# Kernel tuning notes

Hardware: AMD Instinct MI355X
Metric: run time of the kernel (lower is better)

## Reference

```python
import jax, jax.numpy as jnp
import numpy as np

NUM_CLASSES = 100000   # vocab (input_dim of the layer)
DIM = 256              # embedding dim (output_dim of the layer)
BATCH = 256
NUM_TRUE = 1024        # hardcoded num_true in call()
NUM_SAMPLED = 16384    # hardcoded num_sampled in call()
LOG_RANGE = float(np.log(NUM_CLASSES + 1.0))


def _sample_log_uniform_unique(rng, n, range_max):
    # Mimics tf log_uniform_candidate_sampler with unique=True: rejection-sample
    # from P(c) ~ log((c+2)/(c+1)) until n unique ids are collected.
    seen = {}
    log_range = np.log(range_max + 1.0)
    while len(seen) < n:
        u = rng.uniform(0.0, log_range, size=2 * n)
        ids = np.minimum(np.floor(np.exp(u) - 1.0).astype(np.int64), range_max - 1)
        for v in ids.tolist():
            if len(seen) >= n:
                break
            seen[v] = None
    return np.fromiter(seen.keys(), dtype=np.int64, count=n)


def setup_inputs() -> dict:
    key = jax.random.key(0)
    k1, k2, k3, k4 = jax.random.split(key, 4)
    inputs = jax.random.normal(k1, (BATCH, DIM), jnp.float32)
    # Original inits w/b to zeros; use small random values for a non-degenerate baseline.
    w = jax.random.normal(k2, (NUM_CLASSES, DIM), jnp.float32) * 0.02
    b = jax.random.normal(k3, (NUM_CLASSES,), jnp.float32) * 0.02
    labels = jax.random.randint(k4, (BATCH, NUM_TRUE), 0, NUM_CLASSES, dtype=jnp.int32)
    rng = np.random.default_rng(0)
    sampled = jnp.asarray(_sample_log_uniform_unique(rng, NUM_SAMPLED, NUM_CLASSES), jnp.int32)
    return {"inputs": inputs, "w": w, "b": b, "labels": labels, "sampled": sampled}


def _log_uniform_prob(ids):
    idf = ids.astype(jnp.float32)
    return jnp.log((idf + 2.0) / (idf + 1.0)) / LOG_RANGE


def _expected_count(ids):
    # P(id appears among NUM_SAMPLED unique candidates) = 1 - (1-p)^NUM_SAMPLED
    p = _log_uniform_prob(ids)
    return -jnp.expm1(NUM_SAMPLED * jnp.log1p(-p))


def _sigmoid_xent(logits, target):
    # numerically stable sigmoid cross-entropy, target is a scalar label value
    return jnp.maximum(logits, 0.0) - logits * target + jnp.log1p(jnp.exp(-jnp.abs(logits)))


def reference(inputs, w, b, labels, sampled):
    # true logits: per-example dot with each true class row  [B, T]
    true_w = w[labels]                                    # [B, T, D] gather
    true_logits = jnp.einsum('bd,btd->bt', inputs, true_w) + b[labels]
    true_logits = true_logits - jnp.log(_expected_count(labels))
    # sampled logits: shared candidate set  [B, S]
    sampled_logits = inputs @ w[sampled].T + b[sampled]
    sampled_logits = sampled_logits - jnp.log(_expected_count(sampled))
    # NCE targets: 1/num_true for true classes, 0 for sampled; sum over columns
    true_xent = _sigmoid_xent(true_logits, 1.0 / NUM_TRUE)
    sampled_xent = _sigmoid_xent(sampled_logits, 0.0)
    return true_xent.sum(axis=1) + sampled_xent.sum(axis=1)   # [B]
```

## Files before the change

### kernel.cpp

```cpp
#include <hip/hip_runtime.h>
#include <hip/hip_bf16.h>

#define NUM_CLASSES 100000
#define DIM 256
#define BATCH 256
#define NUM_TRUE 1024
#define NUM_SAMPLED 16384
#define LOG_RANGE 11.51293546492023f
#define INV_LOG_RANGE (1.0f / LOG_RANGE)

typedef __bf16 bf16x8 __attribute__((ext_vector_type(8)));
typedef float  f32x4  __attribute__((ext_vector_type(4)));

static __device__ __forceinline__ unsigned short f2bf(float f) {
    unsigned int u = __float_as_uint(f);
    unsigned int lsb = (u >> 16) & 1u;
    u += 0x7fffu + lsb;
    return (unsigned short)(u >> 16);
}

static __device__ __forceinline__ float neg_log_ec(int id) {
    float idf = (float)id;
    float p = logf((idf + 2.0f) / (idf + 1.0f)) * INV_LOG_RANGE;
    float ec = -expm1f((float)NUM_SAMPLED * log1pf(-p));
    return -logf(ec);
}

static __device__ __forceinline__ float dot4(float4 a, float4 b) {
    return fmaf(a.x, b.x, fmaf(a.y, b.y, fmaf(a.z, b.z, a.w * b.w)));
}

__global__ __launch_bounds__(256) void comb_kernel(const float* __restrict__ bias,
                                                   float* __restrict__ comb) {
    int c = blockIdx.x * 256 + threadIdx.x;
    if (c < NUM_CLASSES) comb[c] = bias[c] + neg_log_ec(c);
}

__global__ __launch_bounds__(256) void true_kernel(const float* __restrict__ inputs,
                                                   const float* __restrict__ w,
                                                   const float* __restrict__ comb,
                                                   const int* __restrict__ labels,
                                                   float* __restrict__ out) {
    __shared__ __align__(16) float ins[DIM];
    __shared__ float wsum[4];
    const int tid = threadIdx.x;
    const int b = blockIdx.y;
    ins[tid] = inputs[b * DIM + tid];
    __syncthreads();

    const int lane = tid & 63;
    const int wv   = tid >> 6;
    const int sub  = lane >> 4;
    const int part = lane & 15;
    const float4* ir = (const float4*)ins;
    const float4 in0 = ir[part], in1 = ir[16 + part], in2 = ir[32 + part], in3 = ir[48 + part];

    const int* lab = labels + b * NUM_TRUE + blockIdx.x * 128 + wv * 32;

    float acc = 0.0f;
    float4 w0, w1, w2, w3;
    float cl;
    {
        int l = lab[sub];
        const float4* wr = (const float4*)(w + (size_t)l * DIM);
        w0 = wr[part]; w1 = wr[16 + part]; w2 = wr[32 + part]; w3 = wr[48 + part];
        cl = comb[l];
    }

    #pragma unroll
    for (int i = 0; i < 8; ++i) {
        float4 n0 = {0,0,0,0}, n1 = {0,0,0,0}, n2 = {0,0,0,0}, n3 = {0,0,0,0};
        float cn = 0.0f;
        if (i < 7) {
            int ln = lab[(i + 1) * 4 + sub];
            const float4* wr = (const float4*)(w + (size_t)ln * DIM);
            n0 = wr[part]; n1 = wr[16 + part]; n2 = wr[32 + part]; n3 = wr[48 + part];
            cn = comb[ln];
        }
        float d = dot4(w0, in0) + dot4(w1, in1) + dot4(w2, in2) + dot4(w3, in3);
        d += __shfl_xor(d, 1); d += __shfl_xor(d, 2);
        d += __shfl_xor(d, 4); d += __shfl_xor(d, 8);
        float logit = d + cl;
        float v = fmaxf(logit, 0.0f) - logit * (1.0f / (float)NUM_TRUE)
                + log1pf(expf(-fabsf(logit)));
        acc += (part == 0) ? v : 0.0f;
        w0 = n0; w1 = n1; w2 = n2; w3 = n3; cl = cn;
    }
    acc += __shfl_xor(acc, 16); acc += __shfl_xor(acc, 32);
    if (lane == 0) wsum[wv] = acc;
    __syncthreads();
    if (tid == 0) atomicAdd(&out[b], wsum[0] + wsum[1] + wsum[2] + wsum[3]);
}

#define LWS 264
__global__ __launch_bounds__(256) void sampled_kernel(const float* __restrict__ w,
                                                      const float* __restrict__ comb,
                                                      const int* __restrict__ sampled,
                                                      const float* __restrict__ inputs,
                                                      float* __restrict__ partial) {
    __shared__ unsigned short lw[64][LWS];
    __shared__ unsigned short li[64][LWS];
    __shared__ float cs[64];
    __shared__ float bacc[128];

    const int tid = threadIdx.x;
    const int s0 = blockIdx.x * 64;
    const int bhalf = blockIdx.y;
    if (tid < 128) bacc[tid] = 0.0f;

    const int row = tid & 63;
    const int seg = tid >> 6;
    {
        const int id = sampled[s0 + row];
        const float4* src = (const float4*)(w + (size_t)id * DIM + seg * 64);
        #pragma unroll
        for (int j = 0; j < 16; ++j) {
            float4 v = src[j];
            ushort4 pk;
            pk.x = f2bf(v.x); pk.y = f2bf(v.y); pk.z = f2bf(v.z); pk.w = f2bf(v.w);
            *(ushort4*)(&lw[row][seg * 64 + j * 4]) = pk;
        }
        if (seg == 0) cs[row] = comb[id];
    }

    const int lane = tid & 63;
    const int wv   = tid >> 6;
    const int m    = lane & 15;
    const int quad = lane >> 4;
    const int wy   = wv & 1;
    const int wx   = wv >> 1;

    for (int chunk = 0; chunk < 2; ++chunk) {
        __syncthreads();
        {
            const int bg = bhalf * 128 + chunk * 64 + row;
            const float4* isrc = (const float4*)(inputs + bg * DIM + seg * 64);
            #pragma unroll
            for (int j = 0; j < 16; ++j) {
                float4 v = isrc[j];
                ushort4 pk;
                pk.x = f2bf(v.x); pk.y = f2bf(v.y); pk.z = f2bf(v.z); pk.w = f2bf(v.w);
                *(ushort4*)(&li[row][seg * 64 + j * 4]) = pk;
            }
        }
        __syncthreads();

        f32x4 acc00 = {0,0,0,0}, acc01 = {0,0,0,0}, acc10 = {0,0,0,0}, acc11 = {0,0,0,0};
        const unsigned short* pa0 = &lw[wy * 32 + m][quad * 8];
        const unsigned short* pa1 = &lw[wy * 32 + 16 + m][quad * 8];
        const unsigned short* pb0 = &li[wx * 32 + m][quad * 8];
        const unsigned short* pb1 = &li[wx * 32 + 16 + m][quad * 8];
        #pragma unroll
        for (int kk = 0; kk < 8; ++kk) {
            bf16x8 a0 = *(const bf16x8*)(pa0 + kk * 32);
            bf16x8 a1 = *(const bf16x8*)(pa1 + kk * 32);
            bf16x8 b0 = *(const bf16x8*)(pb0 + kk * 32);
            bf16x8 b1 = *(const bf16x8*)(pb1 + kk * 32);
            acc00 = __builtin_amdgcn_mfma_f32_16x16x32_bf16(a0, b0, acc00, 0, 0, 0);
            acc01 = __builtin_amdgcn_mfma_f32_16x16x32_bf16(a0, b1, acc01, 0, 0, 0);
            acc10 = __builtin_amdgcn_mfma_f32_16x16x32_bf16(a1, b0, acc10, 0, 0, 0);
            acc11 = __builtin_amdgcn_mfma_f32_16x16x32_bf16(a1, b1, acc11, 0, 0, 0);
        }

        float ps0 = 0.0f, ps1 = 0.0f;
        #pragma unroll
        for (int r = 0; r < 4; ++r) {
            {
                float c = cs[wy * 32 + quad * 4 + r];
                float l0 = acc00[r] + c;
                ps0 += fmaxf(l0, 0.0f) + __logf(1.0f + __expf(-fabsf(l0)));
                float l1 = acc01[r] + c;
                ps1 += fmaxf(l1, 0.0f) + __logf(1.0f + __expf(-fabsf(l1)));
            }
            {
                float c = cs[wy * 32 + 16 + quad * 4 + r];
                float l0 = acc10[r] + c;
                ps0 += fmaxf(l0, 0.0f) + __logf(1.0f + __expf(-fabsf(l0)));
                float l1 = acc11[r] + c;
                ps1 += fmaxf(l1, 0.0f) + __logf(1.0f + __expf(-fabsf(l1)));
            }
        }
        ps0 += __shfl_xor(ps0, 16); ps0 += __shfl_xor(ps0, 32);
        ps1 += __shfl_xor(ps1, 16); ps1 += __shfl_xor(ps1, 32);
        if (quad == 0) {
            atomicAdd(&bacc[chunk * 64 + wx * 32 + m], ps0);
            atomicAdd(&bacc[chunk * 64 + wx * 32 + 16 + m], ps1);
        }
    }
    __syncthreads();
    if (tid < 128)
        partial[(bhalf * 256 + blockIdx.x) * 128 + tid] = bacc[tid];
}

__global__ __launch_bounds__(256) void reduce_kernel(const float* __restrict__ partial,
                                                     float* __restrict__ out) {
    __shared__ float wsum[4];
    const int b = blockIdx.x;
    const int tid = threadIdx.x;
    const int y = b >> 7, lb = b & 127;
    float v = partial[(y * 256 + tid) * 128 + lb];
    v += __shfl_xor(v, 1);  v += __shfl_xor(v, 2);  v += __shfl_xor(v, 4);
    v += __shfl_xor(v, 8);  v += __shfl_xor(v, 16); v += __shfl_xor(v, 32);
    if ((tid & 63) == 0) wsum[tid >> 6] = v;
    __syncthreads();
    if (tid == 0) out[b] += wsum[0] + wsum[1] + wsum[2] + wsum[3];
}

extern "C" void kernel_launch(void* const* d_in, const int* in_sizes, int n_in,
                              void* d_out, int out_size, void* d_ws, size_t ws_size,
                              hipStream_t stream) {
    const float* inputs  = (const float*)d_in[0];
    const float* w       = (const float*)d_in[1];
    const float* bias    = (const float*)d_in[2];
    const int*   labels  = (const int*)d_in[3];
    const int*   sampled = (const int*)d_in[4];
    float* out = (float*)d_out;

    float* comb    = (float*)d_ws;
    float* partial = (float*)((char*)d_ws + 409600);

    hipMemsetAsync(out, 0, BATCH * sizeof(float), stream);
    comb_kernel<<<(NUM_CLASSES + 255) / 256, 256, 0, stream>>>(bias, comb);
    true_kernel<<<dim3(8, 256), 256, 0, stream>>>(inputs, w, comb, labels, out);
    sampled_kernel<<<dim3(256, 2), 256, 0, stream>>>(w, comb, sampled, inputs, partial);
    reduce_kernel<<<BATCH, 256, 0, stream>>>(partial, out);
}
```

Baseline: 195.1 us.

## Deepen true-path prefetch, drop memset/atomics, merge sampled batch halves

The true-class kernel now double-buffers two label rows ahead instead of one and uses fast __logf/__expf for the softplus term. Its per-block sums go to a workspace array instead of atomics on the output, and the reduce kernel writes the output directly, so the memset is no longer needed. The sampled kernel now covers all 256 batch rows in one block (4 chunks) instead of splitting the batch across two grid rows. This halves the redundant gather and bf16 conversion of sampled weight rows, at the cost of half as many blocks. Loads use coalesced 16-thread row segments, and the partial layout is transposed so the reduce reads contiguous data.

```diff
diff --git a/kernel.cpp b/kernel.cpp
--- a/kernel.cpp
+++ b/kernel.cpp
@@ -40,7 +40,7 @@
                                                    const float* __restrict__ w,
                                                    const float* __restrict__ comb,
                                                    const int* __restrict__ labels,
-                                                   float* __restrict__ out) {
+                                                   float* __restrict__ truep) {
     __shared__ __align__(16) float ins[DIM];
     __shared__ float wsum[4];
     const int tid = threadIdx.x;
@@ -57,39 +57,42 @@
 
     const int* lab = labels + b * NUM_TRUE + blockIdx.x * 128 + wv * 32;
 
+    float4 buf[2][4];
+    float  cb[2];
+    #pragma unroll
+    for (int s = 0; s < 2; ++s) {
+        int l = lab[s * 4 + sub];
+        const float4* wr = (const float4*)(w + (size_t)l * DIM);
+        buf[s][0] = wr[part];      buf[s][1] = wr[16 + part];
+        buf[s][2] = wr[32 + part]; buf[s][3] = wr[48 + part];
+        cb[s] = comb[l];
+    }
+
     float acc = 0.0f;
-    float4 w0, w1, w2, w3;
-    float cl;
-    {
-        int l = lab[sub];
-        const float4* wr = (const float4*)(w + (size_t)l * DIM);
-        w0 = wr[part]; w1 = wr[16 + part]; w2 = wr[32 + part]; w3 = wr[48 + part];
-        cl = comb[l];
-    }
-
     #pragma unroll
     for (int i = 0; i < 8; ++i) {
-        float4 n0 = {0,0,0,0}, n1 = {0,0,0,0}, n2 = {0,0,0,0}, n3 = {0,0,0,0};
-        float cn = 0.0f;
-        if (i < 7) {
-            int ln = lab[(i + 1) * 4 + sub];
-            const float4* wr = (const float4*)(w + (size_t)ln * DIM);
-            n0 = wr[part]; n1 = wr[16 + part]; n2 = wr[32 + part]; n3 = wr[48 + part];
-            cn = comb[ln];
+        const int cur = i & 1;
+        float4 w0 = buf[cur][0], w1 = buf[cur][1], w2 = buf[cur][2], w3 = buf[cur][3];
+        float cl = cb[cur];
+        if (i < 6) {
+            int l = lab[(i + 2) * 4 + sub];
+            const float4* wr = (const float4*)(w + (size_t)l * DIM);
+            buf[cur][0] = wr[part];      buf[cur][1] = wr[16 + part];
+            buf[cur][2] = wr[32 + part]; buf[cur][3] = wr[48 + part];
+            cb[cur] = comb[l];
         }
         float d = dot4(w0, in0) + dot4(w1, in1) + dot4(w2, in2) + dot4(w3, in3);
         d += __shfl_xor(d, 1); d += __shfl_xor(d, 2);
         d += __shfl_xor(d, 4); d += __shfl_xor(d, 8);
         float logit = d + cl;
         float v = fmaxf(logit, 0.0f) - logit * (1.0f / (float)NUM_TRUE)
-                + log1pf(expf(-fabsf(logit)));
+                + __logf(1.0f + __expf(-fabsf(logit)));
         acc += (part == 0) ? v : 0.0f;
-        w0 = n0; w1 = n1; w2 = n2; w3 = n3; cl = cn;
     }
     acc += __shfl_xor(acc, 16); acc += __shfl_xor(acc, 32);
     if (lane == 0) wsum[wv] = acc;
     __syncthreads();
-    if (tid == 0) atomicAdd(&out[b], wsum[0] + wsum[1] + wsum[2] + wsum[3]);
+    if (tid == 0) truep[b * 8 + blockIdx.x] = wsum[0] + wsum[1] + wsum[2] + wsum[3];
 }
 
 #define LWS 264
@@ -101,27 +104,29 @@
     __shared__ unsigned short lw[64][LWS];
     __shared__ unsigned short li[64][LWS];
     __shared__ float cs[64];
-    __shared__ float bacc[128];
+    __shared__ float bacc[BATCH];
 
     const int tid = threadIdx.x;
     const int s0 = blockIdx.x * 64;
-    const int bhalf = blockIdx.y;
-    if (tid < 128) bacc[tid] = 0.0f;
-
-    const int row = tid & 63;
-    const int seg = tid >> 6;
-    {
-        const int id = sampled[s0 + row];
-        const float4* src = (const float4*)(w + (size_t)id * DIM + seg * 64);
-        #pragma unroll
-        for (int j = 0; j < 16; ++j) {
-            float4 v = src[j];
+    bacc[tid] = 0.0f;
+
+    const int inner = tid & 15;
+    const int r16   = tid >> 4;
+
+    #pragma unroll
+    for (int rb = 0; rb < 4; ++rb) {
+        const int r = rb * 16 + r16;
+        const int id = sampled[s0 + r];
+        const float* src = w + (size_t)id * DIM;
+        #pragma unroll
+        for (int j = 0; j < 4; ++j) {
+            float4 v = *(const float4*)(src + j * 64 + inner * 4);
             ushort4 pk;
             pk.x = f2bf(v.x); pk.y = f2bf(v.y); pk.z = f2bf(v.z); pk.w = f2bf(v.w);
-            *(ushort4*)(&lw[row][seg * 64 + j * 4]) = pk;
-        }
-        if (seg == 0) cs[row] = comb[id];
-    }
+            *(ushort4*)(&lw[r][j * 64 + inner * 4]) = pk;
+        }
+    }
+    if (tid < 64) cs[tid] = comb[sampled[s0 + tid]];
 
     const int lane = tid & 63;
     const int wv   = tid >> 6;
@@ -130,17 +135,18 @@
     const int wy   = wv & 1;
     const int wx   = wv >> 1;
 
-    for (int chunk = 0; chunk < 2; ++chunk) {
+    for (int chunk = 0; chunk < 4; ++chunk) {
         __syncthreads();
-        {
-            const int bg = bhalf * 128 + chunk * 64 + row;
-            const float4* isrc = (const float4*)(inputs + bg * DIM + seg * 64);
+        #pragma unroll
+        for (int rb = 0; rb < 4; ++rb) {
+            const int r = rb * 16 + r16;
+            const float* src = inputs + (size_t)(chunk * 64 + r) * DIM;
             #pragma unroll
-            for (int j = 0; j < 16; ++j) {
-                float4 v = isrc[j];
+            for (int j = 0; j < 4; ++j) {
+                float4 v = *(const float4*)(src + j * 64 + inner * 4);
                 ushort4 pk;
                 pk.x = f2bf(v.x); pk.y = f2bf(v.y); pk.z = f2bf(v.z); pk.w = f2bf(v.w);
-                *(ushort4*)(&li[row][seg * 64 + j * 4]) = pk;
+                *(ushort4*)(&li[r][j * 64 + inner * 4]) = pk;
             }
         }
         __syncthreads();
@@ -188,22 +194,22 @@
         }
     }
     __syncthreads();
-    if (tid < 128)
-        partial[(bhalf * 256 + blockIdx.x) * 128 + tid] = bacc[tid];
+    partial[tid * 256 + blockIdx.x] = bacc[tid];
 }
 
 __global__ __launch_bounds__(256) void reduce_kernel(const float* __restrict__ partial,
+                                                     const float* __restrict__ truep,
                                                      float* __restrict__ out) {
     __shared__ float wsum[4];
     const int b = blockIdx.x;
     const int tid = threadIdx.x;
-    const int y = b >> 7, lb = b & 127;
-    float v = partial[(y * 256 + tid) * 128 + lb];
+    float v = partial[b * 256 + tid];
+    if (tid < 8) v += truep[b * 8 + tid];
     v += __shfl_xor(v, 1);  v += __shfl_xor(v, 2);  v += __shfl_xor(v, 4);
     v += __shfl_xor(v, 8);  v += __shfl_xor(v, 16); v += __shfl_xor(v, 32);
     if ((tid & 63) == 0) wsum[tid >> 6] = v;
     __syncthreads();
-    if (tid == 0) out[b] += wsum[0] + wsum[1] + wsum[2] + wsum[3];
+    if (tid == 0) out[b] = wsum[0] + wsum[1] + wsum[2] + wsum[3];
 }
 
 extern "C" void kernel_launch(void* const* d_in, const int* in_sizes, int n_in,
@@ -217,11 +223,11 @@
     float* out = (float*)d_out;
 
     float* comb    = (float*)d_ws;
-    float* partial = (float*)((char*)d_ws + 409600);
-
-    hipMemsetAsync(out, 0, BATCH * sizeof(float), stream);
+    float* truep   = (float*)((char*)d_ws + 409600);
+    float* partial = (float*)((char*)d_ws + 417792);
+
     comb_kernel<<<(NUM_CLASSES + 255) / 256, 256, 0, stream>>>(bias, comb);
-    true_kernel<<<dim3(8, 256), 256, 0, stream>>>(inputs, w, comb, labels, out);
-    sampled_kernel<<<dim3(256, 2), 256, 0, stream>>>(w, comb, sampled, inputs, partial);
-    reduce_kernel<<<BATCH, 256, 0, stream>>>(partial, out);
-}
+    true_kernel<<<dim3(8, 256), 256, 0, stream>>>(inputs, w, comb, labels, truep);
+    sampled_kernel<<<256, 256, 0, stream>>>(w, comb, sampled, inputs, partial);
+    reduce_kernel<<<BATCH, 256, 0, stream>>>(partial, truep, out);
+}
```

Result: faster. 189.6 us (-2.8%).
